# Kernel optimization log

Measured on AMD Instinct MI355X. Metric: run time of the kernel, lower is better.

Reference implementation:

```python
import jax, jax.numpy as jnp
import numpy as np

NUM_OBJECTS = 6          # self.NUM_OBJECTS
SCORE_THRESH = 1e-4      # self.score_tresh
NMS_THRESHS = jnp.asarray(np.arange(0.001, 1.0, 0.1), dtype=jnp.float32)  # 10 thresholds
K_CAND = 1024            # fixed-shape cap on (proposal,class) candidates per image
CLASS_OFFSET = 4096.0    # > max image coord; batched_nms per-class offset trick


def _iou_matrix(b):
    # b: [K,4] xyxy -> [K,K] IoU
    x1, y1, x2, y2 = b[:, 0], b[:, 1], b[:, 2], b[:, 3]
    area = (x2 - x1) * (y2 - y1)
    iw = jnp.clip(jnp.minimum(x2[:, None], x2[None, :]) - jnp.maximum(x1[:, None], x1[None, :]), 0.0)
    ih = jnp.clip(jnp.minimum(y2[:, None], y2[None, :]) - jnp.maximum(y1[:, None], y1[None, :]), 0.0)
    inter = iw * ih
    union = area[:, None] + area[None, :] - inter
    return jnp.where(union > 0, inter / union, 0.0)


def _greedy_nms(iou, valid, thresh):
    # candidates are pre-sorted by descending score; sequential greedy suppression
    K = valid.shape[0]
    ar = jnp.arange(K)
    def body(i, keep):
        sup = keep[i] & (iou[i] > thresh) & (ar > i)
        return keep & ~sup
    return jax.lax.fori_loop(0, K, body, valid)


def _per_image(logits, boxes, feats, hw):
    # logits [N,81], boxes [N,80,4], feats [N,2048], hw [2] (h,w)
    C = boxes.shape[1]
    probs = jax.nn.softmax(logits, axis=-1)[:, :C]          # drop background class
    h = hw[0].astype(boxes.dtype)
    w = hw[1].astype(boxes.dtype)
    b = jnp.stack([jnp.clip(boxes[..., 0], 0.0, w),         # clip to image
                   jnp.clip(boxes[..., 1], 0.0, h),
                   jnp.clip(boxes[..., 2], 0.0, w),
                   jnp.clip(boxes[..., 3], 0.0, h)], axis=-1)
    scores = probs.reshape(-1)                              # [N*C]
    vals, idx = jax.lax.top_k(jnp.where(scores > SCORE_THRESH, scores, -1.0), K_CAND)
    cand_valid = vals > SCORE_THRESH
    cb = b.reshape(-1, 4)[idx]                              # [K,4]
    cls = (idx % C).astype(boxes.dtype)
    prop = idx // C                                         # proposal row index
    iou = _iou_matrix(cb + cls[:, None] * CLASS_OFFSET)     # per-class NMS via offsets
    keeps = jax.vmap(lambda t: _greedy_nms(iou, cand_valid, t))(NMS_THRESHS)  # [T,K]
    counts = keeps.sum(axis=1)
    # torch loop: break at first (smallest) thresh yielding len(ids)==6, i.e. >=6 kept
    ok = counts >= NUM_OBJECTS
    t_sel = jnp.where(jnp.any(ok), jnp.argmax(ok), NMS_THRESHS.shape[0] - 1)
    keep = keeps[t_sel]
    _, top = jax.lax.top_k(jnp.where(keep, vals, -jnp.inf), NUM_OBJECTS)
    ids = prop[top]                                         # [6]
    return feats[ids].T                                     # [2048, 6] (permute(1,0))


def _forward(cls_logits, boxes, feature_pooled, image_hw):
    return jax.vmap(_per_image)(cls_logits, boxes, feature_pooled, image_hw)  # [B,2048,6]


def setup_inputs() -> dict:
    key = jax.random.key(0)
    k1, k2, k3, k4, k5 = jax.random.split(key, 5)
    B, N, C, D = 8, 1000, 80, 2048
    cls_logits = jax.random.normal(k1, (B, N, C + 1), dtype=jnp.float32)
    ctr = jax.random.uniform(k2, (B, N, C, 2), minval=0.0, maxval=800.0)
    sz = jax.random.uniform(k3, (B, N, C, 2), minval=8.0, maxval=200.0)
    boxes = jnp.concatenate([ctr - sz * 0.5, ctr + sz * 0.5], axis=-1).astype(jnp.float32)
    feature_pooled = jax.random.normal(k4, (B, N, D), dtype=jnp.float32)
    image_hw = jax.random.randint(k5, (B, 2), 600, 800, dtype=jnp.int32)
    return {"cls_logits": cls_logits, "boxes": boxes,
            "feature_pooled": feature_pooled, "image_hw": image_hw}


def reference(cls_logits, boxes, feature_pooled, image_hw):
    return _forward(cls_logits, boxes, feature_pooled, image_hw)
```

## Files before the change

kernel.cpp:

```cpp
#include <hip/hip_runtime.h>
#include <cmath>
#include <cstdint>

#define NB 8
#define NPROP 1000
#define NCLS 80
#define NLOG 81
#define KCAND 1024
#define NTH 10
#define DFEAT 2048
#define NOBJ 6
#define NSCORE (NPROP*NCLS)
#define HBLK 8
#define HCHUNK (NSCORE/HBLK)
#define PCHUNK (NPROP/HBLK)
#define CCAP 64

constexpr size_t OFF_SCORES = 0;
constexpr size_t SZ_SCORES  = (size_t)NB * NSCORE * 4;
constexpr size_t OFF_LISTA  = OFF_SCORES + SZ_SCORES;
constexpr size_t SZ_LISTA   = (size_t)NB * 20 * KCAND * 8;
constexpr size_t OFF_H1     = OFF_LISTA;
constexpr size_t OFF_H2     = OFF_H1 + (size_t)NB * HBLK * 2048 * 4;
constexpr size_t OFF_PIV    = OFF_H2 + (size_t)NB * HBLK * 2048 * 4;
constexpr size_t OFF_CBUF   = OFF_PIV + (size_t)NB * 8 * 4;
constexpr size_t OFF_CANDK  = OFF_LISTA + SZ_LISTA;
constexpr size_t SZ_CANDK   = (size_t)NB * KCAND * 8;
constexpr size_t OFF_CX1    = OFF_CANDK + SZ_CANDK;
constexpr size_t SZ_CARR    = (size_t)NB * KCAND * 4;
constexpr size_t OFF_CY1    = OFF_CX1 + SZ_CARR;
constexpr size_t OFF_CX2    = OFF_CY1 + SZ_CARR;
constexpr size_t OFF_CY2    = OFF_CX2 + SZ_CARR;
constexpr size_t OFF_CAREA  = OFF_CY2 + SZ_CARR;
constexpr size_t OFF_CPROP  = OFF_CAREA + SZ_CARR;
constexpr size_t OFF_VALIDW = OFF_CPROP + SZ_CARR;
constexpr size_t SZ_VALIDW  = (size_t)NB * 16 * 8;
constexpr size_t OFF_CCNT   = OFF_VALIDW + SZ_VALIDW;
constexpr size_t OFF_CLIST  = OFF_CCNT + (size_t)NB * NCLS * 4;
constexpr size_t OFF_KEEPS  = OFF_CLIST + (size_t)NB * NCLS * CCAP * 4;
constexpr size_t SZ_KEEPS   = (size_t)NB * NTH * 16 * 8;

__device__ __forceinline__ float nms_th(int t) {
    return (float)(0.001 + 0.1 * (double)t);
}

__device__ __forceinline__ unsigned score_vkey(float v) {
    float vv = (v > 1e-4f) ? v : -1.0f;
    unsigned bits = __float_as_uint(vv);
    unsigned u = (bits & 0x80000000u) ? ~bits : (bits | 0x80000000u);
    return ~u;
}

__global__ __launch_bounds__(1024) void k_softhist(const float* __restrict__ logits,
                                                   float* __restrict__ scores,
                                                   unsigned* __restrict__ hist1) {
    __shared__ unsigned hh[2048];
    int img = blockIdx.x >> 3, blk = blockIdx.x & 7;
    int tid = threadIdx.x, wid = tid >> 6, lane = tid & 63;
    hh[tid] = 0; hh[tid + 1024] = 0;
    __syncthreads();
    for (int p = wid; p < PCHUNK; p += 16) {
        int prop = blk * PCHUNK + p;
        const float* L = logits + ((size_t)img * NPROP + prop) * NLOG;
        float l0 = L[lane];
        float l1 = (lane < 17) ? L[64 + lane] : -INFINITY;
        float m = fmaxf(l0, l1);
        #pragma unroll
        for (int o = 32; o > 0; o >>= 1) m = fmaxf(m, __shfl_xor(m, o, 64));
        float e0 = expf(l0 - m);
        float e1 = (lane < 17) ? expf(l1 - m) : 0.f;
        float s = e0 + e1;
        #pragma unroll
        for (int o = 32; o > 0; o >>= 1) s += __shfl_xor(s, o, 64);
        float* op = scores + ((size_t)img * NPROP + prop) * NCLS;
        float p0 = e0 / s;
        op[lane] = p0;
        atomicAdd(&hh[score_vkey(p0) >> 21], 1u);
        if (lane < 16) {
            float p1 = e1 / s;
            op[64 + lane] = p1;
            atomicAdd(&hh[score_vkey(p1) >> 21], 1u);
        }
    }
    __syncthreads();
    unsigned* outp = hist1 + ((size_t)img * HBLK + blk) * 2048;
    outp[tid] = hh[tid];
    outp[tid + 1024] = hh[tid + 1024];
}

__device__ __forceinline__ void pivot_scan(const unsigned* __restrict__ h8, unsigned K,
                                           int* __restrict__ out_b, int* __restrict__ out_rem) {
    __shared__ unsigned wsum[16];
    int tid = threadIdx.x;
    unsigned a = 0, b = 0;
    #pragma unroll
    for (int s = 0; s < HBLK; ++s) {
        a += h8[s * 2048 + 2 * tid];
        b += h8[s * 2048 + 2 * tid + 1];
    }
    unsigned p = a + b;
    unsigned x = p;
    #pragma unroll
    for (int d = 1; d < 64; d <<= 1) {
        unsigned y = __shfl_up(x, (unsigned)d, 64);
        if ((tid & 63) >= d) x += y;
    }
    if ((tid & 63) == 63) wsum[tid >> 6] = x;
    __syncthreads();
    if (tid < 16) {
        unsigned w = wsum[tid];
        #pragma unroll
        for (int d = 1; d < 16; d <<= 1) {
            unsigned y = __shfl_up(w, (unsigned)d, 64);
            if (tid >= d) w += y;
        }
        wsum[tid] = w;
    }
    __syncthreads();
    unsigned wex = (tid >= 64) ? wsum[(tid >> 6) - 1] : 0u;
    unsigned incl = x + wex;
    unsigned E = incl - p;
    if (E < K && E + a >= K)              { *out_b = 2 * tid;     *out_rem = (int)(K - E); }
    else if (E + a < K && E + a + b >= K) { *out_b = 2 * tid + 1; *out_rem = (int)(K - (E + a)); }
}

__global__ __launch_bounds__(1024) void k_hist2p(const float* __restrict__ scores,
                                                 const unsigned* __restrict__ hist1,
                                                 unsigned* __restrict__ hist2,
                                                 int* __restrict__ piv) {
    __shared__ unsigned hh[2048];
    __shared__ int sb, sr;
    int img = blockIdx.x >> 3, blk = blockIdx.x & 7;
    int tid = threadIdx.x;
    hh[tid] = 0; hh[tid + 1024] = 0;
    pivot_scan(hist1 + (size_t)img * HBLK * 2048, KCAND, &sb, &sr);
    __syncthreads();
    unsigned b1 = (unsigned)sb;
    const float* sc = scores + (size_t)img * NSCORE + (size_t)blk * HCHUNK;
    for (int e = tid; e < HCHUNK; e += 1024) {
        unsigned vk = score_vkey(sc[e]);
        if ((vk >> 21) == b1) atomicAdd(&hh[(vk >> 10) & 2047u], 1u);
    }
    __syncthreads();
    unsigned* outp = hist2 + ((size_t)img * HBLK + blk) * 2048;
    outp[tid] = hh[tid];
    outp[tid + 1024] = hh[tid + 1024];
    if (blk == 0 && tid == 0) {
        piv[img * 8 + 0] = sb;
        piv[img * 8 + 1] = sr;
        piv[img * 8 + 3] = 0;
    }
}

__global__ __launch_bounds__(1024) void k_gatherp(const float* __restrict__ scores,
                                                  const unsigned* __restrict__ hist2,
                                                  int* __restrict__ piv,
                                                  unsigned long long* __restrict__ cbuf,
                                                  int* __restrict__ ccnt,
                                                  unsigned long long* __restrict__ validw,
                                                  unsigned long long* __restrict__ keeps) {
    __shared__ int sb2, sr2;
    __shared__ unsigned lcnt, gbase;
    int img = blockIdx.x >> 3, blk = blockIdx.x & 7;
    int tid = threadIdx.x;
    if (blockIdx.x == 0) {
        if (tid < NB * NCLS) ccnt[tid] = 0;
        if (tid >= 640 && tid < 640 + NB * 16) validw[tid - 640] = 0ULL;
    }
    if (blockIdx.x == 1) {
        for (int k = tid; k < NB * NTH * 16; k += 1024) keeps[k] = 0ULL;
    }
    if (tid == 0) lcnt = 0;
    unsigned K2 = (unsigned)piv[img * 8 + 1];
    pivot_scan(hist2 + (size_t)img * HBLK * 2048, K2, &sb2, &sr2);
    __syncthreads();
    unsigned T22 = ((unsigned)piv[img * 8 + 0] << 11) | (unsigned)sb2;
    const float* sc = scores + (size_t)img * NSCORE + (size_t)blk * HCHUNK;
    unsigned long long sel[(HCHUNK + 1023) / 1024];
    int ns = 0;
    for (int e = tid; e < HCHUNK; e += 1024) {
        unsigned vk = score_vkey(sc[e]);
        if ((vk >> 10) <= T22)
            sel[ns++] = ((unsigned long long)vk << 32) | (unsigned)(blk * HCHUNK + e);
    }
    unsigned lp = atomicAdd(&lcnt, (unsigned)ns);
    __syncthreads();
    if (tid == 0) gbase = atomicAdd((unsigned*)&piv[img * 8 + 3], lcnt);
    __syncthreads();
    unsigned long long* ob = cbuf + (size_t)img * 2048;
    for (int i = 0; i < ns; ++i) {
        unsigned pos = gbase + lp + (unsigned)i;
        if (pos < 2048) ob[pos] = sel[i];
    }
}

__global__ __launch_bounds__(256) void k_rankcand(const unsigned long long* __restrict__ cbuf,
                                                  const int* __restrict__ piv,
                                                  const float* __restrict__ boxes,
                                                  const int* __restrict__ hw,
                                                  float* __restrict__ cx1, float* __restrict__ cy1,
                                                  float* __restrict__ cx2, float* __restrict__ cy2,
                                                  float* __restrict__ car, int* __restrict__ cprop,
                                                  unsigned long long* __restrict__ validw,
                                                  int* __restrict__ ccnt, int* __restrict__ clist) {
    __shared__ unsigned long long keys[2048];
    int img = blockIdx.x >> 3, sl = blockIdx.x & 7;
    int tid = threadIdx.x;
    int cnt = piv[img * 8 + 3]; if (cnt > 2048) cnt = 2048;
    const unsigned long long* ib = cbuf + (size_t)img * 2048;
    #pragma unroll
    for (int k = 0; k < 8; ++k) {
        int t = k * 256 + tid;
        keys[t] = (t < cnt) ? ib[t] : ~0ULL;
    }
    __syncthreads();
    unsigned long long a = keys[sl * 256 + tid];
    int r = 0;
    #pragma unroll 8
    for (int j = 0; j < cnt; ++j) r += (keys[j] < a) ? 1 : 0;
    if (sl * 256 + tid < cnt && r < KCAND) {
        unsigned u   = ~(unsigned)(a >> 32);
        unsigned idx = (unsigned)a;
        const unsigned uth = __float_as_uint(1e-4f) | 0x80000000u;
        bool valid = u > uth;
        int prop = (int)(idx / NCLS);
        int cls  = (int)(idx - (unsigned)prop * NCLS);
        const float4 bx = *(const float4*)(boxes + ((((size_t)img * NPROP + prop) * NCLS + cls) << 2));
        float h = (float)hw[img * 2 + 0];
        float w = (float)hw[img * 2 + 1];
        float x1 = fminf(fmaxf(bx.x, 0.f), w);
        float y1 = fminf(fmaxf(bx.y, 0.f), h);
        float x2 = fminf(fmaxf(bx.z, 0.f), w);
        float y2 = fminf(fmaxf(bx.w, 0.f), h);
        float offc = __fmul_rn((float)cls, 4096.0f);
        x1 = __fadd_rn(x1, offc); y1 = __fadd_rn(y1, offc);
        x2 = __fadd_rn(x2, offc); y2 = __fadd_rn(y2, offc);
        float area = __fmul_rn(__fsub_rn(x2, x1), __fsub_rn(y2, y1));
        int o = img * KCAND + r;
        cx1[o] = x1; cy1[o] = y1; cx2[o] = x2; cy2[o] = y2;
        car[o] = area; cprop[o] = prop;
        if (valid) atomicOr(&validw[img * 16 + (r >> 6)], 1ULL << (r & 63));
        int slot = atomicAdd(&ccnt[img * NCLS + cls], 1);
        if (slot < CCAP) clist[(img * NCLS + cls) * CCAP + slot] = r;
    }
}

__global__ __launch_bounds__(256) void k_cnms(const int* __restrict__ ccnt,
                                              const int* __restrict__ clist,
                                              const float* __restrict__ cx1,
                                              const float* __restrict__ cy1,
                                              const float* __restrict__ cx2,
                                              const float* __restrict__ cy2,
                                              const float* __restrict__ car,
                                              const unsigned long long* __restrict__ validw,
                                              unsigned long long* __restrict__ keeps) {
    int gid  = blockIdx.x * 4 + (threadIdx.x >> 6);
    int lane = threadIdx.x & 63;
    if (gid >= NB * NCLS) return;
    int img = gid / NCLS, cls = gid - img * NCLS;
    int n = ccnt[img * NCLS + cls];
    if (n > CCAP) n = CCAP;
    if (n == 0) return;
    int r = (lane < n) ? clist[(img * NCLS + cls) * CCAP + lane] : 0x7fffffff;
    int pos = 0;
    for (int j = 0; j < n; ++j) {
        int rj = __shfl(r, j, 64);
        pos += (rj < r) ? 1 : 0;
    }
    int srt = 0;
    for (int j = 0; j < n; ++j) {
        int pj = __shfl(pos, j, 64);
        int rj = __shfl(r, j, 64);
        if (pj == lane) srt = rj;
    }
    bool act = lane < n;
    int base = img * KCAND;
    float x1 = 0, y1 = 0, x2 = 0, y2 = 0, ar = 0;
    bool val = false;
    if (act) {
        x1 = cx1[base + srt]; y1 = cy1[base + srt];
        x2 = cx2[base + srt]; y2 = cy2[base + srt]; ar = car[base + srt];
        val = (validw[img * 16 + (srt >> 6)] >> (srt & 63)) & 1ULL;
    }
    unsigned long long m[NTH];
    #pragma unroll
    for (int t = 0; t < NTH; ++t) m[t] = 0ULL;
    for (int b = 0; b < n; ++b) {
        float xj1 = __shfl(x1, b, 64), yj1 = __shfl(y1, b, 64);
        float xj2 = __shfl(x2, b, 64), yj2 = __shfl(y2, b, 64);
        float aj  = __shfl(ar, b, 64);
        float iw = fmaxf(__fsub_rn(fminf(x2, xj2), fmaxf(x1, xj1)), 0.f);
        float ih = fmaxf(__fsub_rn(fminf(y2, yj2), fmaxf(y1, yj1)), 0.f);
        float inter = __fmul_rn(iw, ih);
        float uni   = __fsub_rn(__fadd_rn(ar, aj), inter);
        float iou   = (uni > 0.f) ? __fdiv_rn(inter, uni) : 0.f;
        if (act && b < lane) {
            #pragma unroll
            for (int t = 0; t < NTH; ++t)
                if (iou > nms_th(t)) m[t] |= 1ULL << b;
        }
    }
    unsigned long long vmask = __ballot(act && val);
    for (int t = 0; t < NTH; ++t) {
        unsigned long long keep = vmask;
        for (int it = 0; it <= n; ++it) {
            bool nk = act && val && ((m[t] & keep) == 0ULL);
            unsigned long long nb = __ballot(nk);
            if (nb == keep) break;
            keep = nb;
        }
        if (act && ((keep >> lane) & 1ULL))
            atomicOr(&keeps[((size_t)img * NTH + t) * 16 + (srt >> 6)], 1ULL << (srt & 63));
    }
}

__global__ __launch_bounds__(256) void k_selfeat(const unsigned long long* __restrict__ keeps,
                                                 const int* __restrict__ cprop,
                                                 const float* __restrict__ feats,
                                                 float* __restrict__ outp) {
    __shared__ int scnt[NTH];
    __shared__ unsigned long long skw[16];
    __shared__ int stsel;
    __shared__ int sids[NOBJ];
    int img = blockIdx.x >> 3;
    int tid = threadIdx.x;
    if (tid < NTH) scnt[tid] = 0;
    __syncthreads();
    if (tid < NTH * 16) {
        unsigned long long w = keeps[(size_t)img * NTH * 16 + tid];
        int pc = __popcll(w);
        if (pc) atomicAdd(&scnt[tid >> 4], pc);
    }
    __syncthreads();
    if (tid == 0) {
        int tsel = NTH - 1;
        for (int t = 0; t < NTH; ++t) if (scnt[t] >= NOBJ) { tsel = t; break; }
        stsel = tsel;
    }
    __syncthreads();
    if (tid < 16) skw[tid] = keeps[((size_t)img * NTH + stsel) * 16 + tid];
    __syncthreads();
    if (tid == 0) {
        int got = 0;
        for (int k = 0; k < 16 && got < NOBJ; ++k) {
            unsigned long long x = skw[k];
            while (x && got < NOBJ) {
                int b = __builtin_ctzll(x);
                sids[got++] = cprop[img * KCAND + k * 64 + b];
                x &= x - 1;
            }
        }
        for (int k = 0; k < 16 && got < NOBJ; ++k) {
            unsigned long long x = ~skw[k];
            while (x && got < NOBJ) {
                int b = __builtin_ctzll(x);
                sids[got++] = cprop[img * KCAND + k * 64 + b];
                x &= x - 1;
            }
        }
    }
    __syncthreads();
    int d = (blockIdx.x & 7) * 256 + tid;
    const float* fb = feats + (size_t)img * NPROP * DFEAT;
    float* ob = outp + ((size_t)img * DFEAT + d) * NOBJ;
    #pragma unroll
    for (int s = 0; s < NOBJ; ++s)
        ob[s] = fb[(size_t)sids[s] * DFEAT + d];
}

extern "C" void kernel_launch(void* const* d_in, const int* in_sizes, int n_in,
                              void* d_out, int out_size, void* d_ws, size_t ws_size,
                              hipStream_t stream) {
    const float* logits = (const float*)d_in[0];
    const float* boxes  = (const float*)d_in[1];
    const float* feats  = (const float*)d_in[2];
    const int*   hw     = (const int*)d_in[3];
    float* outp = (float*)d_out;

    char* ws = (char*)d_ws;
    float*              scores = (float*)(ws + OFF_SCORES);
    unsigned*           hist1  = (unsigned*)(ws + OFF_H1);
    unsigned*           hist2  = (unsigned*)(ws + OFF_H2);
    int*                piv    = (int*)(ws + OFF_PIV);
    unsigned long long* cbuf   = (unsigned long long*)(ws + OFF_CBUF);
    float* cx1 = (float*)(ws + OFF_CX1);
    float* cy1 = (float*)(ws + OFF_CY1);
    float* cx2 = (float*)(ws + OFF_CX2);
    float* cy2 = (float*)(ws + OFF_CY2);
    float* car = (float*)(ws + OFF_CAREA);
    int*   cprop = (int*)(ws + OFF_CPROP);
    unsigned long long* validw = (unsigned long long*)(ws + OFF_VALIDW);
    int*   ccnt  = (int*)(ws + OFF_CCNT);
    int*   clist = (int*)(ws + OFF_CLIST);
    unsigned long long* keeps  = (unsigned long long*)(ws + OFF_KEEPS);

    k_softhist<<<NB * HBLK, 1024, 0, stream>>>(logits, scores, hist1);
    k_hist2p<<<NB * HBLK, 1024, 0, stream>>>(scores, hist1, hist2, piv);
    k_gatherp<<<NB * HBLK, 1024, 0, stream>>>(scores, hist2, piv, cbuf, ccnt, validw, keeps);
    k_rankcand<<<NB * HBLK, 256, 0, stream>>>(cbuf, piv, boxes, hw,
                                              cx1, cy1, cx2, cy2, car, cprop,
                                              validw, ccnt, clist);
    k_cnms<<<(NB * NCLS + 3) / 4, 256, 0, stream>>>(ccnt, clist, cx1, cy1, cx2, cy2,
                                                    car, validw, keeps);
    k_selfeat<<<NB * HBLK, 256, 0, stream>>>(keeps, cprop, feats, outp);
}
```

Before: 163.6 us.

## Fuse per-image select, rank, NMS and gather into one block kernel

Result: slower. 205.1 us (+25.4%).

```diff
diff --git a/kernel.cpp b/kernel.cpp
--- a/kernel.cpp
+++ b/kernel.cpp
@@ -12,33 +12,30 @@
 #define NOBJ 6
 #define NSCORE (NPROP*NCLS)
 #define HBLK 8
-#define HCHUNK (NSCORE/HBLK)
 #define PCHUNK (NPROP/HBLK)
 #define CCAP 64
+#define GMAX 2048
 
 constexpr size_t OFF_SCORES = 0;
 constexpr size_t SZ_SCORES  = (size_t)NB * NSCORE * 4;
-constexpr size_t OFF_LISTA  = OFF_SCORES + SZ_SCORES;
-constexpr size_t SZ_LISTA   = (size_t)NB * 20 * KCAND * 8;
-constexpr size_t OFF_H1     = OFF_LISTA;
-constexpr size_t OFF_H2     = OFF_H1 + (size_t)NB * HBLK * 2048 * 4;
-constexpr size_t OFF_PIV    = OFF_H2 + (size_t)NB * HBLK * 2048 * 4;
-constexpr size_t OFF_CBUF   = OFF_PIV + (size_t)NB * 8 * 4;
-constexpr size_t OFF_CANDK  = OFF_LISTA + SZ_LISTA;
-constexpr size_t SZ_CANDK   = (size_t)NB * KCAND * 8;
-constexpr size_t OFF_CX1    = OFF_CANDK + SZ_CANDK;
-constexpr size_t SZ_CARR    = (size_t)NB * KCAND * 4;
-constexpr size_t OFF_CY1    = OFF_CX1 + SZ_CARR;
-constexpr size_t OFF_CX2    = OFF_CY1 + SZ_CARR;
-constexpr size_t OFF_CY2    = OFF_CX2 + SZ_CARR;
-constexpr size_t OFF_CAREA  = OFF_CY2 + SZ_CARR;
-constexpr size_t OFF_CPROP  = OFF_CAREA + SZ_CARR;
-constexpr size_t OFF_VALIDW = OFF_CPROP + SZ_CARR;
-constexpr size_t SZ_VALIDW  = (size_t)NB * 16 * 8;
-constexpr size_t OFF_CCNT   = OFF_VALIDW + SZ_VALIDW;
-constexpr size_t OFF_CLIST  = OFF_CCNT + (size_t)NB * NCLS * 4;
-constexpr size_t OFF_KEEPS  = OFF_CLIST + (size_t)NB * NCLS * CCAP * 4;
-constexpr size_t SZ_KEEPS   = (size_t)NB * NTH * 16 * 8;
+constexpr size_t OFF_H1     = OFF_SCORES + SZ_SCORES;
+
+constexpr int L_KEYS  = 0;
+constexpr int L_S1P   = L_KEYS  + 2048 * 8;
+constexpr int L_S2P   = L_S1P   + 2048 * 4;
+constexpr int L_HH    = L_S2P   + 2048 * 4;
+constexpr int L_GCNT  = L_HH    + 2048 * 4;
+constexpr int L_CX1   = L_GCNT  + 4096 * 4;
+constexpr int L_CY1   = L_CX1   + KCAND * 4;
+constexpr int L_CX2   = L_CY1   + KCAND * 4;
+constexpr int L_CY2   = L_CX2   + KCAND * 4;
+constexpr int L_CAR   = L_CY2   + KCAND * 4;
+constexpr int L_CPROP = L_CAR   + KCAND * 4;
+constexpr int L_CLIST = L_CPROP + KCAND * 4;
+constexpr int L_CCNT  = L_CLIST + NCLS * CCAP * 4;
+constexpr int L_VALID = L_CCNT  + NCLS * 4;
+constexpr int L_KEEPS = L_VALID + 16 * 8;
+constexpr int SMEM_BYTES = L_KEEPS + NTH * 16 * 8;
 
 __device__ __forceinline__ float nms_th(int t) {
     return (float)(0.001 + 0.1 * (double)t);
@@ -88,16 +85,10 @@
     outp[tid + 1024] = hh[tid + 1024];
 }
 
-__device__ __forceinline__ void pivot_scan(const unsigned* __restrict__ h8, unsigned K,
-                                           int* __restrict__ out_b, int* __restrict__ out_rem) {
+__device__ __forceinline__ void scan2048(unsigned a, unsigned b, unsigned* pre,
+                                         unsigned K, int* out_b, int* out_rem) {
     __shared__ unsigned wsum[16];
     int tid = threadIdx.x;
-    unsigned a = 0, b = 0;
-    #pragma unroll
-    for (int s = 0; s < HBLK; ++s) {
-        a += h8[s * 2048 + 2 * tid];
-        b += h8[s * 2048 + 2 * tid + 1];
-    }
     unsigned p = a + b;
     unsigned x = p;
     #pragma unroll
@@ -118,227 +109,213 @@
     }
     __syncthreads();
     unsigned wex = (tid >= 64) ? wsum[(tid >> 6) - 1] : 0u;
-    unsigned incl = x + wex;
-    unsigned E = incl - p;
+    unsigned E = x + wex - p;
+    pre[2 * tid]     = E;
+    pre[2 * tid + 1] = E + a;
     if (E < K && E + a >= K)              { *out_b = 2 * tid;     *out_rem = (int)(K - E); }
     else if (E + a < K && E + a + b >= K) { *out_b = 2 * tid + 1; *out_rem = (int)(K - (E + a)); }
 }
 
-__global__ __launch_bounds__(1024) void k_hist2p(const float* __restrict__ scores,
-                                                 const unsigned* __restrict__ hist1,
-                                                 unsigned* __restrict__ hist2,
-                                                 int* __restrict__ piv) {
-    __shared__ unsigned hh[2048];
-    __shared__ int sb, sr;
-    int img = blockIdx.x >> 3, blk = blockIdx.x & 7;
-    int tid = threadIdx.x;
-    hh[tid] = 0; hh[tid + 1024] = 0;
-    pivot_scan(hist1 + (size_t)img * HBLK * 2048, KCAND, &sb, &sr);
-    __syncthreads();
-    unsigned b1 = (unsigned)sb;
-    const float* sc = scores + (size_t)img * NSCORE + (size_t)blk * HCHUNK;
-    for (int e = tid; e < HCHUNK; e += 1024) {
-        unsigned vk = score_vkey(sc[e]);
-        if ((vk >> 21) == b1) atomicAdd(&hh[(vk >> 10) & 2047u], 1u);
-    }
-    __syncthreads();
-    unsigned* outp = hist2 + ((size_t)img * HBLK + blk) * 2048;
-    outp[tid] = hh[tid];
-    outp[tid + 1024] = hh[tid + 1024];
-    if (blk == 0 && tid == 0) {
-        piv[img * 8 + 0] = sb;
-        piv[img * 8 + 1] = sr;
-        piv[img * 8 + 3] = 0;
-    }
-}
-
-__global__ __launch_bounds__(1024) void k_gatherp(const float* __restrict__ scores,
-                                                  const unsigned* __restrict__ hist2,
-                                                  int* __restrict__ piv,
-                                                  unsigned long long* __restrict__ cbuf,
-                                                  int* __restrict__ ccnt,
-                                                  unsigned long long* __restrict__ validw,
-                                                  unsigned long long* __restrict__ keeps) {
-    __shared__ int sb2, sr2;
-    __shared__ unsigned lcnt, gbase;
-    int img = blockIdx.x >> 3, blk = blockIdx.x & 7;
-    int tid = threadIdx.x;
-    if (blockIdx.x == 0) {
-        if (tid < NB * NCLS) ccnt[tid] = 0;
-        if (tid >= 640 && tid < 640 + NB * 16) validw[tid - 640] = 0ULL;
-    }
-    if (blockIdx.x == 1) {
-        for (int k = tid; k < NB * NTH * 16; k += 1024) keeps[k] = 0ULL;
-    }
-    if (tid == 0) lcnt = 0;
-    unsigned K2 = (unsigned)piv[img * 8 + 1];
-    pivot_scan(hist2 + (size_t)img * HBLK * 2048, K2, &sb2, &sr2);
-    __syncthreads();
-    unsigned T22 = ((unsigned)piv[img * 8 + 0] << 11) | (unsigned)sb2;
-    const float* sc = scores + (size_t)img * NSCORE + (size_t)blk * HCHUNK;
-    unsigned long long sel[(HCHUNK + 1023) / 1024];
-    int ns = 0;
-    for (int e = tid; e < HCHUNK; e += 1024) {
-        unsigned vk = score_vkey(sc[e]);
-        if ((vk >> 10) <= T22)
-            sel[ns++] = ((unsigned long long)vk << 32) | (unsigned)(blk * HCHUNK + e);
-    }
-    unsigned lp = atomicAdd(&lcnt, (unsigned)ns);
-    __syncthreads();
-    if (tid == 0) gbase = atomicAdd((unsigned*)&piv[img * 8 + 3], lcnt);
-    __syncthreads();
-    unsigned long long* ob = cbuf + (size_t)img * 2048;
-    for (int i = 0; i < ns; ++i) {
-        unsigned pos = gbase + lp + (unsigned)i;
-        if (pos < 2048) ob[pos] = sel[i];
-    }
-}
-
-__global__ __launch_bounds__(256) void k_rankcand(const unsigned long long* __restrict__ cbuf,
-                                                  const int* __restrict__ piv,
-                                                  const float* __restrict__ boxes,
-                                                  const int* __restrict__ hw,
-                                                  float* __restrict__ cx1, float* __restrict__ cy1,
-                                                  float* __restrict__ cx2, float* __restrict__ cy2,
-                                                  float* __restrict__ car, int* __restrict__ cprop,
-                                                  unsigned long long* __restrict__ validw,
-                                                  int* __restrict__ ccnt, int* __restrict__ clist) {
-    __shared__ unsigned long long keys[2048];
-    int img = blockIdx.x >> 3, sl = blockIdx.x & 7;
-    int tid = threadIdx.x;
-    int cnt = piv[img * 8 + 3]; if (cnt > 2048) cnt = 2048;
-    const unsigned long long* ib = cbuf + (size_t)img * 2048;
-    #pragma unroll
-    for (int k = 0; k < 8; ++k) {
-        int t = k * 256 + tid;
-        keys[t] = (t < cnt) ? ib[t] : ~0ULL;
-    }
-    __syncthreads();
-    unsigned long long a = keys[sl * 256 + tid];
-    int r = 0;
-    #pragma unroll 8
-    for (int j = 0; j < cnt; ++j) r += (keys[j] < a) ? 1 : 0;
-    if (sl * 256 + tid < cnt && r < KCAND) {
-        unsigned u   = ~(unsigned)(a >> 32);
-        unsigned idx = (unsigned)a;
-        const unsigned uth = __float_as_uint(1e-4f) | 0x80000000u;
-        bool valid = u > uth;
-        int prop = (int)(idx / NCLS);
-        int cls  = (int)(idx - (unsigned)prop * NCLS);
-        const float4 bx = *(const float4*)(boxes + ((((size_t)img * NPROP + prop) * NCLS + cls) << 2));
-        float h = (float)hw[img * 2 + 0];
-        float w = (float)hw[img * 2 + 1];
-        float x1 = fminf(fmaxf(bx.x, 0.f), w);
-        float y1 = fminf(fmaxf(bx.y, 0.f), h);
-        float x2 = fminf(fmaxf(bx.z, 0.f), w);
-        float y2 = fminf(fmaxf(bx.w, 0.f), h);
-        float offc = __fmul_rn((float)cls, 4096.0f);
-        x1 = __fadd_rn(x1, offc); y1 = __fadd_rn(y1, offc);
-        x2 = __fadd_rn(x2, offc); y2 = __fadd_rn(y2, offc);
-        float area = __fmul_rn(__fsub_rn(x2, x1), __fsub_rn(y2, y1));
-        int o = img * KCAND + r;
-        cx1[o] = x1; cy1[o] = y1; cx2[o] = x2; cy2[o] = y2;
-        car[o] = area; cprop[o] = prop;
-        if (valid) atomicOr(&validw[img * 16 + (r >> 6)], 1ULL << (r & 63));
-        int slot = atomicAdd(&ccnt[img * NCLS + cls], 1);
-        if (slot < CCAP) clist[(img * NCLS + cls) * CCAP + slot] = r;
-    }
-}
-
-__global__ __launch_bounds__(256) void k_cnms(const int* __restrict__ ccnt,
-                                              const int* __restrict__ clist,
-                                              const float* __restrict__ cx1,
-                                              const float* __restrict__ cy1,
-                                              const float* __restrict__ cx2,
-                                              const float* __restrict__ cy2,
-                                              const float* __restrict__ car,
-                                              const unsigned long long* __restrict__ validw,
-                                              unsigned long long* __restrict__ keeps) {
-    int gid  = blockIdx.x * 4 + (threadIdx.x >> 6);
-    int lane = threadIdx.x & 63;
-    if (gid >= NB * NCLS) return;
-    int img = gid / NCLS, cls = gid - img * NCLS;
-    int n = ccnt[img * NCLS + cls];
-    if (n > CCAP) n = CCAP;
-    if (n == 0) return;
-    int r = (lane < n) ? clist[(img * NCLS + cls) * CCAP + lane] : 0x7fffffff;
-    int pos = 0;
-    for (int j = 0; j < n; ++j) {
-        int rj = __shfl(r, j, 64);
-        pos += (rj < r) ? 1 : 0;
-    }
-    int srt = 0;
-    for (int j = 0; j < n; ++j) {
-        int pj = __shfl(pos, j, 64);
-        int rj = __shfl(r, j, 64);
-        if (pj == lane) srt = rj;
-    }
-    bool act = lane < n;
-    int base = img * KCAND;
-    float x1 = 0, y1 = 0, x2 = 0, y2 = 0, ar = 0;
-    bool val = false;
-    if (act) {
-        x1 = cx1[base + srt]; y1 = cy1[base + srt];
-        x2 = cx2[base + srt]; y2 = cy2[base + srt]; ar = car[base + srt];
-        val = (validw[img * 16 + (srt >> 6)] >> (srt & 63)) & 1ULL;
-    }
-    unsigned long long m[NTH];
-    #pragma unroll
-    for (int t = 0; t < NTH; ++t) m[t] = 0ULL;
-    for (int b = 0; b < n; ++b) {
-        float xj1 = __shfl(x1, b, 64), yj1 = __shfl(y1, b, 64);
-        float xj2 = __shfl(x2, b, 64), yj2 = __shfl(y2, b, 64);
-        float aj  = __shfl(ar, b, 64);
-        float iw = fmaxf(__fsub_rn(fminf(x2, xj2), fmaxf(x1, xj1)), 0.f);
-        float ih = fmaxf(__fsub_rn(fminf(y2, yj2), fmaxf(y1, yj1)), 0.f);
-        float inter = __fmul_rn(iw, ih);
-        float uni   = __fsub_rn(__fadd_rn(ar, aj), inter);
-        float iou   = (uni > 0.f) ? __fdiv_rn(inter, uni) : 0.f;
-        if (act && b < lane) {
-            #pragma unroll
-            for (int t = 0; t < NTH; ++t)
-                if (iou > nms_th(t)) m[t] |= 1ULL << b;
-        }
-    }
-    unsigned long long vmask = __ballot(act && val);
-    for (int t = 0; t < NTH; ++t) {
-        unsigned long long keep = vmask;
-        for (int it = 0; it <= n; ++it) {
-            bool nk = act && val && ((m[t] & keep) == 0ULL);
-            unsigned long long nb = __ballot(nk);
-            if (nb == keep) break;
-            keep = nb;
-        }
-        if (act && ((keep >> lane) & 1ULL))
-            atomicOr(&keeps[((size_t)img * NTH + t) * 16 + (srt >> 6)], 1ULL << (srt & 63));
-    }
-}
-
-__global__ __launch_bounds__(256) void k_selfeat(const unsigned long long* __restrict__ keeps,
-                                                 const int* __restrict__ cprop,
-                                                 const float* __restrict__ feats,
-                                                 float* __restrict__ outp) {
-    __shared__ int scnt[NTH];
+__global__ __launch_bounds__(1024) void k_image(const float* __restrict__ scores,
+                                                const unsigned* __restrict__ hist1,
+                                                const float* __restrict__ boxes,
+                                                const int* __restrict__ hw,
+                                                const float* __restrict__ feats,
+                                                float* __restrict__ outp) {
+    extern __shared__ char smem[];
+    unsigned long long* keys2 = (unsigned long long*)(smem + L_KEYS);
+    unsigned* s1p   = (unsigned*)(smem + L_S1P);
+    unsigned* s2p   = (unsigned*)(smem + L_S2P);
+    unsigned* hh    = (unsigned*)(smem + L_HH);
+    unsigned* gcnt  = (unsigned*)(smem + L_GCNT);
+    float* scx1     = (float*)(smem + L_CX1);
+    float* scy1     = (float*)(smem + L_CY1);
+    float* scx2     = (float*)(smem + L_CX2);
+    float* scy2     = (float*)(smem + L_CY2);
+    float* scar     = (float*)(smem + L_CAR);
+    int*   scprop   = (int*)(smem + L_CPROP);
+    int*   sclist   = (int*)(smem + L_CLIST);
+    int*   sccnt    = (int*)(smem + L_CCNT);
+    unsigned long long* svalid = (unsigned long long*)(smem + L_VALID);
+    unsigned long long* skeeps = (unsigned long long*)(smem + L_KEEPS);
+
+    __shared__ int sb1, sr1, sb2, sr2;
+    __shared__ int scnt6[NTH];
     __shared__ unsigned long long skw[16];
     __shared__ int stsel;
     __shared__ int sids[NOBJ];
-    int img = blockIdx.x >> 3;
+
+    int img = blockIdx.x;
     int tid = threadIdx.x;
-    if (tid < NTH) scnt[tid] = 0;
-    __syncthreads();
+
+    hh[tid] = 0; hh[tid + 1024] = 0;
+    gcnt[tid] = 0; gcnt[tid + 1024] = 0; gcnt[tid + 2048] = 0; gcnt[tid + 3072] = 0;
+    scprop[tid] = 0;
+    if (tid < NCLS) sccnt[tid] = 0;
+    if (tid < 16) svalid[tid] = 0ULL;
+    if (tid < NTH * 16) skeeps[tid] = 0ULL;
+    if (tid < NTH) scnt6[tid] = 0;
+
+    unsigned a1 = 0, b1v = 0;
+    const unsigned* h1 = hist1 + (size_t)img * HBLK * 2048;
+    #pragma unroll
+    for (int s = 0; s < HBLK; ++s) {
+        a1  += h1[s * 2048 + 2 * tid];
+        b1v += h1[s * 2048 + 2 * tid + 1];
+    }
+    scan2048(a1, b1v, s1p, KCAND, &sb1, &sr1);
+    __syncthreads();
+
+    unsigned b1 = (unsigned)sb1;
+    const float* sc = scores + (size_t)img * NSCORE;
+    const float4* sc4 = (const float4*)sc;
+    #define H2(val) { unsigned vk = score_vkey(val); \
+                      if ((vk >> 21) == b1) atomicAdd(&hh[(vk >> 10) & 2047u], 1u); }
+    for (int e4 = tid; e4 < NSCORE / 4; e4 += 1024) {
+        float4 v = sc4[e4];
+        H2(v.x) H2(v.y) H2(v.z) H2(v.w)
+    }
+    #undef H2
+    __syncthreads();
+    scan2048(hh[2 * tid], hh[2 * tid + 1], s2p, (unsigned)sr1, &sb2, &sr2);
+    __syncthreads();
+
+    unsigned T22 = (b1 << 11) | (unsigned)sb2;
+    #define GA(val, ei) { unsigned vk = score_vkey(val); unsigned t22 = vk >> 10; \
+        if (t22 <= T22) { \
+            unsigned h = vk >> 21; unsigned g, base; \
+            if (h == b1) { unsigned sub = t22 & 2047u; g = 2048u + sub; base = s1p[b1] + s2p[sub]; } \
+            else         { g = h;                      base = s1p[h]; } \
+            unsigned slot = atomicAdd(&gcnt[g], 1u); \
+            unsigned posn = base + slot; \
+            if (posn < GMAX) keys2[posn] = ((unsigned long long)vk << 32) | (unsigned)(ei); } }
+    for (int e4 = tid; e4 < NSCORE / 4; e4 += 1024) {
+        float4 v = sc4[e4];
+        int e = 4 * e4;
+        GA(v.x, e) GA(v.y, e + 1) GA(v.z, e + 2) GA(v.w, e + 3)
+    }
+    #undef GA
+    __syncthreads();
+
+    int cnt = (int)(s1p[b1] + s2p[(unsigned)sb2] + gcnt[2048u + (unsigned)sb2]);
+    if (cnt > GMAX) cnt = GMAX;
+    for (int p = tid; p < cnt; p += 1024) {
+        unsigned long long akey = keys2[p];
+        unsigned vk = (unsigned)(akey >> 32);
+        unsigned h = vk >> 21;
+        unsigned base, gsz;
+        if (h == b1) {
+            unsigned sub = (vk >> 10) & 2047u;
+            base = s1p[b1] + s2p[sub];
+            gsz  = gcnt[2048u + sub];
+        } else {
+            base = s1p[h];
+            gsz  = gcnt[h];
+        }
+        int r = (int)base;
+        unsigned qe = base + gsz; if (qe > (unsigned)GMAX) qe = (unsigned)GMAX;
+        for (unsigned q = base; q < qe; ++q)
+            r += (keys2[q] < akey) ? 1 : 0;
+        if (r < KCAND) {
+            unsigned u   = ~vk;
+            unsigned idx = (unsigned)akey;
+            const unsigned uth = __float_as_uint(1e-4f) | 0x80000000u;
+            bool valid = u > uth;
+            int prop = (int)(idx / NCLS);
+            int cls  = (int)(idx - (unsigned)prop * NCLS);
+            const float4 bx = *(const float4*)(boxes + ((((size_t)img * NPROP + prop) * NCLS + cls) << 2));
+            float fh = (float)hw[img * 2 + 0];
+            float fw = (float)hw[img * 2 + 1];
+            float x1 = fminf(fmaxf(bx.x, 0.f), fw);
+            float y1 = fminf(fmaxf(bx.y, 0.f), fh);
+            float x2 = fminf(fmaxf(bx.z, 0.f), fw);
+            float y2 = fminf(fmaxf(bx.w, 0.f), fh);
+            float offc = __fmul_rn((float)cls, 4096.0f);
+            x1 = __fadd_rn(x1, offc); y1 = __fadd_rn(y1, offc);
+            x2 = __fadd_rn(x2, offc); y2 = __fadd_rn(y2, offc);
+            float area = __fmul_rn(__fsub_rn(x2, x1), __fsub_rn(y2, y1));
+            scx1[r] = x1; scy1[r] = y1; scx2[r] = x2; scy2[r] = y2;
+            scar[r] = area; scprop[r] = prop;
+            if (valid) atomicOr(&svalid[r >> 6], 1ULL << (r & 63));
+            int slot = atomicAdd(&sccnt[cls], 1);
+            if (slot < CCAP) sclist[cls * CCAP + slot] = r;
+        }
+    }
+    __syncthreads();
+
+    {
+        int wv = tid >> 6, lane = tid & 63;
+        for (int cls = wv; cls < NCLS; cls += 16) {
+            int n = sccnt[cls];
+            if (n > CCAP) n = CCAP;
+            if (n == 0) continue;
+            int rk = (lane < n) ? sclist[cls * CCAP + lane] : 0x7fffffff;
+            int pos = 0;
+            for (int j = 0; j < n; ++j) {
+                int rj = __shfl(rk, j, 64);
+                pos += (rj < rk) ? 1 : 0;
+            }
+            int srt = 0;
+            for (int j = 0; j < n; ++j) {
+                int pj = __shfl(pos, j, 64);
+                int rj = __shfl(rk, j, 64);
+                if (pj == lane) srt = rj;
+            }
+            bool act = lane < n;
+            float x1 = 0, y1 = 0, x2 = 0, y2 = 0, ar = 0;
+            bool val = false;
+            if (act) {
+                x1 = scx1[srt]; y1 = scy1[srt];
+                x2 = scx2[srt]; y2 = scy2[srt]; ar = scar[srt];
+                val = (svalid[srt >> 6] >> (srt & 63)) & 1ULL;
+            }
+            unsigned long long m[NTH];
+            #pragma unroll
+            for (int t = 0; t < NTH; ++t) m[t] = 0ULL;
+            for (int b = 0; b < n; ++b) {
+                float xj1 = __shfl(x1, b, 64), yj1 = __shfl(y1, b, 64);
+                float xj2 = __shfl(x2, b, 64), yj2 = __shfl(y2, b, 64);
+                float aj  = __shfl(ar, b, 64);
+                float iw = fmaxf(__fsub_rn(fminf(x2, xj2), fmaxf(x1, xj1)), 0.f);
+                float ih = fmaxf(__fsub_rn(fminf(y2, yj2), fmaxf(y1, yj1)), 0.f);
+                float inter = __fmul_rn(iw, ih);
+                float uni   = __fsub_rn(__fadd_rn(ar, aj), inter);
+                float iou   = (uni > 0.f) ? __fdiv_rn(inter, uni) : 0.f;
+                if (act && b < lane) {
+                    #pragma unroll
+                    for (int t = 0; t < NTH; ++t)
+                        if (iou > nms_th(t)) m[t] |= 1ULL << b;
+                }
+            }
+            unsigned long long vmask = __ballot(act && val);
+            for (int t = 0; t < NTH; ++t) {
+                unsigned long long keep = vmask;
+                for (int it = 0; it <= n; ++it) {
+                    bool nk = act && val && ((m[t] & keep) == 0ULL);
+                    unsigned long long nb = __ballot(nk);
+                    if (nb == keep) break;
+                    keep = nb;
+                }
+                if (act && ((keep >> lane) & 1ULL))
+                    atomicOr(&skeeps[t * 16 + (srt >> 6)], 1ULL << (srt & 63));
+            }
+        }
+    }
+    __syncthreads();
+
     if (tid < NTH * 16) {
-        unsigned long long w = keeps[(size_t)img * NTH * 16 + tid];
+        unsigned long long w = skeeps[tid];
         int pc = __popcll(w);
-        if (pc) atomicAdd(&scnt[tid >> 4], pc);
+        if (pc) atomicAdd(&scnt6[tid >> 4], pc);
     }
     __syncthreads();
     if (tid == 0) {
         int tsel = NTH - 1;
-        for (int t = 0; t < NTH; ++t) if (scnt[t] >= NOBJ) { tsel = t; break; }
+        for (int t = 0; t < NTH; ++t) if (scnt6[t] >= NOBJ) { tsel = t; break; }
         stsel = tsel;
     }
     __syncthreads();
-    if (tid < 16) skw[tid] = keeps[((size_t)img * NTH + stsel) * 16 + tid];
+    if (tid < 16) skw[tid] = skeeps[stsel * 16 + tid];
     __syncthreads();
     if (tid == 0) {
         int got = 0;
@@ -346,7 +323,7 @@
             unsigned long long x = skw[k];
             while (x && got < NOBJ) {
                 int b = __builtin_ctzll(x);
-                sids[got++] = cprop[img * KCAND + k * 64 + b];
+                sids[got++] = scprop[k * 64 + b];
                 x &= x - 1;
             }
         }
@@ -354,18 +331,19 @@
             unsigned long long x = ~skw[k];
             while (x && got < NOBJ) {
                 int b = __builtin_ctzll(x);
-                sids[got++] = cprop[img * KCAND + k * 64 + b];
+                sids[got++] = scprop[k * 64 + b];
                 x &= x - 1;
             }
         }
     }
     __syncthreads();
-    int d = (blockIdx.x & 7) * 256 + tid;
     const float* fb = feats + (size_t)img * NPROP * DFEAT;
-    float* ob = outp + ((size_t)img * DFEAT + d) * NOBJ;
-    #pragma unroll
-    for (int s = 0; s < NOBJ; ++s)
-        ob[s] = fb[(size_t)sids[s] * DFEAT + d];
+    for (int d = tid; d < DFEAT; d += 1024) {
+        float* ob = outp + ((size_t)img * DFEAT + d) * NOBJ;
+        #pragma unroll
+        for (int s = 0; s < NOBJ; ++s)
+            ob[s] = fb[(size_t)sids[s] * DFEAT + d];
+    }
 }
 
 extern "C" void kernel_launch(void* const* d_in, const int* in_sizes, int n_in,
@@ -378,29 +356,17 @@
     float* outp = (float*)d_out;
 
     char* ws = (char*)d_ws;
-    float*              scores = (float*)(ws + OFF_SCORES);
-    unsigned*           hist1  = (unsigned*)(ws + OFF_H1);
-    unsigned*           hist2  = (unsigned*)(ws + OFF_H2);
-    int*                piv    = (int*)(ws + OFF_PIV);
-    unsigned long long* cbuf   = (unsigned long long*)(ws + OFF_CBUF);
-    float* cx1 = (float*)(ws + OFF_CX1);
-    float* cy1 = (float*)(ws + OFF_CY1);
-    float* cx2 = (float*)(ws + OFF_CX2);
-    float* cy2 = (float*)(ws + OFF_CY2);
-    float* car = (float*)(ws + OFF_CAREA);
-    int*   cprop = (int*)(ws + OFF_CPROP);
-    unsigned long long* validw = (unsigned long long*)(ws + OFF_VALIDW);
-    int*   ccnt  = (int*)(ws + OFF_CCNT);
-    int*   clist = (int*)(ws + OFF_CLIST);
-    unsigned long long* keeps  = (unsigned long long*)(ws + OFF_KEEPS);
+    float*    scores = (float*)(ws + OFF_SCORES);
+    unsigned* hist1  = (unsigned*)(ws + OFF_H1);
+
+    static bool attr_done = false;
+    if (!attr_done) {
+        (void)hipFuncSetAttribute(reinterpret_cast<const void*>(&k_image),
+                                  hipFuncAttributeMaxDynamicSharedMemorySize,
+                                  SMEM_BYTES);
+        attr_done = true;
+    }
 
     k_softhist<<<NB * HBLK, 1024, 0, stream>>>(logits, scores, hist1);
-    k_hist2p<<<NB * HBLK, 1024, 0, stream>>>(scores, hist1, hist2, piv);
-    k_gatherp<<<NB * HBLK, 1024, 0, stream>>>(scores, hist2, piv, cbuf, ccnt, validw, keeps);
-    k_rankcand<<<NB * HBLK, 256, 0, stream>>>(cbuf, piv, boxes, hw,
-                                              cx1, cy1, cx2, cy2, car, cprop,
-                                              validw, ccnt, clist);
-    k_cnms<<<(NB * NCLS + 3) / 4, 256, 0, stream>>>(ccnt, clist, cx1, cy1, cx2, cy2,
-                                                    car, validw, keeps);
-    k_selfeat<<<NB * HBLK, 256, 0, stream>>>(keeps, cprop, feats, outp);
-}
+    k_image<<<NB, 1024, SMEM_BYTES, stream>>>(scores, hist1, boxes, hw, feats, outp);
+}
```
